# Kernel optimization log

Hardware: AMD Instinct MI355X
Metric: run time of the kernel (lower is better)

The kernel has to match this reference:

```python
import jax, jax.numpy as jnp
import numpy as np

B, T, E = 2, 4096, 768
H, Dh = 12, 64
W = 256  # one-sided window
GLOBAL_IDX = np.arange(0, 4096, 256)  # 16 global token positions
G = GLOBAL_IDX.shape[0]
NEG = -1e9


def setup_inputs() -> dict:
    key = jax.random.key(0)
    ks = jax.random.split(key, 13)
    p = lambda k, shape: jax.random.normal(k, shape, dtype=jnp.float32) * 0.02
    inp = {"x": jax.random.normal(ks[0], (B, T, E), dtype=jnp.float32)}
    for n_i, n in enumerate(["q", "k", "v", "qg", "kg", "vg"]):
        inp["W" + n] = p(ks[1 + 2 * n_i], (E, E))
        inp["b" + n] = p(ks[2 + 2 * n_i], (E,))
    return inp


def _heads(t):
    # [B,T,E] -> [B,H,T,Dh]
    return t.reshape(B, -1, H, Dh).transpose(0, 2, 1, 3)


def _chunk(t, w):
    # [B,H,T,d] -> [B,H,nc,3w,d]: key/value chunks covering [c*w - w, c*w + 2w)
    nc = T // w
    tp = jnp.pad(t, ((0, 0), (0, 0), (w, w), (0, 0)))
    idx = jnp.arange(nc)[:, None] * w + jnp.arange(3 * w)[None, :]
    return tp[:, :, idx, :]


def _forward(x, Wq, bq, Wk, bk, Wv, bv, Wqg, bqg, Wkg, bkg, Wvg, bvg):
    scale = 1.0 / np.sqrt(Dh)
    q = _heads(x @ Wq + bq) * scale
    k = _heads(x @ Wk + bk)
    v = _heads(x @ Wv + bv)
    nc = T // W
    qc = q.reshape(B, H, nc, W, Dh)
    kc = _chunk(k, W)
    vc = _chunk(v, W)
    # banded local scores via 3-chunk trick: [B,H,nc,W,3W]
    scores = jnp.einsum('bhcid,bhcjd->bhcij', qc, kc)
    i = jnp.arange(W)
    j = jnp.arange(3 * W)
    band = (j[None, :] >= i[:, None]) & (j[None, :] <= i[:, None] + 2 * W)  # |diff|<=W
    key_pos = jnp.arange(nc)[:, None] * W + j[None, :] - W  # [nc,3W] absolute key pos
    inseq = (key_pos >= 0) & (key_pos < T)
    valid = band[None] & inseq[:, None, :]  # [nc,W,3W]
    # remove global tokens from windowed attention (float -10000 mask, HF-style)
    is_glob = jnp.zeros((T,), jnp.float32).at[jnp.asarray(GLOBAL_IDX)].set(1.0)
    gmask = is_glob[jnp.clip(key_pos, 0, T - 1)] * inseq
    scores = scores - 10000.0 * gmask[None, None, :, None, :]
    scores = jnp.where(valid[None, None], scores, NEG)
    # every query also attends to global keys (local k/v projections gathered)
    k_glob = k[:, :, GLOBAL_IDX, :]  # [B,H,G,Dh]
    v_glob = v[:, :, GLOBAL_IDX, :]
    gscores = jnp.einsum('bhcid,bhgd->bhcig', qc, k_glob)  # [B,H,nc,W,G]
    allp = jax.nn.softmax(jnp.concatenate([gscores, scores], axis=-1), axis=-1)
    pg = allp[..., :G]
    pl = allp[..., G:] * valid[None, None]
    out = (jnp.einsum('bhcij,bhcjd->bhcid', pl, vc)
           + jnp.einsum('bhcig,bhgd->bhcid', pg, v_glob))
    out = out.reshape(B, H, T, Dh).transpose(0, 2, 1, 3).reshape(B, T, E)
    # global-query tokens: full attention with global projections, overwrite rows
    xg = x[:, GLOBAL_IDX, :]  # [B,G,E]
    qg = (xg @ Wqg + bqg).reshape(B, G, H, Dh).transpose(0, 2, 1, 3) * scale
    kgl = _heads(x @ Wkg + bkg)
    vgl = _heads(x @ Wvg + bvg)
    gp = jax.nn.softmax(jnp.einsum('bhgd,bhtd->bhgt', qg, kgl), axis=-1)
    go = jnp.einsum('bhgt,bhtd->bhgd', gp, vgl).transpose(0, 2, 1, 3).reshape(B, G, E)
    return out.at[:, GLOBAL_IDX, :].set(go)


def reference(x, Wq, bq, Wk, bk, Wv, bv, Wqg, bqg, Wkg, bkg, Wvg, bvg):
    return _forward(x, Wq, bq, Wk, bk, Wv, bv, Wqg, bqg, Wkg, bkg, Wvg, bvg)
```

## Files before the change

### kernel.cpp

```cpp
#include <hip/hip_runtime.h>
#include <stdint.h>
#include <stddef.h>

#define BB 2
#define TT 4096
#define EE 768
#define HH 12
#define DH 64
#define WW 256
#define NCHUNK 16
#define GG 16

typedef __bf16 bf16_t;
typedef __bf16 bf16x8 __attribute__((ext_vector_type(8)));
typedef float f32x4 __attribute__((ext_vector_type(4)));

__device__ inline f32x4 mfma16(bf16x8 a, bf16x8 b, f32x4 c) {
    return __builtin_amdgcn_mfma_f32_16x16x32_bf16(a, b, c, 0, 0, 0);
}

__device__ inline void gload16(const void* g, void* l) {
    __builtin_amdgcn_global_load_lds(
        (const __attribute__((address_space(1))) void*)g,
        (__attribute__((address_space(3))) void*)l, 16, 0, 0);
}

__global__ __launch_bounds__(256) void k_prep(const float* __restrict__ x,
                                              bf16_t* __restrict__ xb,
                                              const float* __restrict__ w0,
                                              const float* __restrict__ w1,
                                              const float* __restrict__ w2,
                                              const float* __restrict__ w3,
                                              const float* __restrict__ w4,
                                              bf16_t* __restrict__ wt) {
    __shared__ __align__(16) bf16_t ls[64 * 65];
    const int tid = threadIdx.x;
    if (blockIdx.x < 3072) {
        const int i = (blockIdx.x * 256 + tid) * 8;
        f32x4 a = *(const f32x4*)(x + i);
        f32x4 b = *(const f32x4*)(x + i + 4);
        bf16x8 o;
        o[0] = (bf16_t)a[0]; o[1] = (bf16_t)a[1]; o[2] = (bf16_t)a[2]; o[3] = (bf16_t)a[3];
        o[4] = (bf16_t)b[0]; o[5] = (bf16_t)b[1]; o[6] = (bf16_t)b[2]; o[7] = (bf16_t)b[3];
        *(bf16x8*)(xb + i) = o;
    } else {
        const int idx0 = blockIdx.x - 3072;
        const int z = idx0 / 144;
        const int rr = idx0 % 144;
        const int k0 = (rr / 12) * 64;
        const int n0 = (rr % 12) * 64;
        const float* W = (z == 0) ? w0 : (z == 1) ? w1 : (z == 2) ? w2 : (z == 3) ? w3 : w4;
        #pragma unroll
        for (int i = 0; i < 16; ++i) {
            int idx = i * 256 + tid;
            int kr = idx >> 6, nc = idx & 63;
            ls[nc * 65 + kr] = (bf16_t)W[(size_t)(k0 + kr) * EE + n0 + nc];
        }
        __syncthreads();
        bf16_t* o = wt + (size_t)z * EE * EE;
        #pragma unroll
        for (int i = 0; i < 16; ++i) {
            int idx = i * 256 + tid;
            int nr = idx >> 6, kc = idx & 63;
            o[(size_t)(n0 + nr) * EE + k0 + kc] = ls[nr * 65 + kc];
        }
    }
}

__global__ __launch_bounds__(256) void k_gemm(const bf16_t* __restrict__ xb,
                                              const bf16_t* __restrict__ wt,
                                              const float* __restrict__ b0,
                                              const float* __restrict__ b1,
                                              const float* __restrict__ b2,
                                              const float* __restrict__ b3,
                                              const float* __restrict__ b4,
                                              bf16_t* __restrict__ proj,
                                              bf16_t* __restrict__ vTp) {
    const int tid = threadIdx.x;
    const int z = blockIdx.z;
    const int m0 = blockIdx.x * 128;
    const int n0 = blockIdx.y * 128;
    const float* bias = (z == 0) ? b0 : (z == 1) ? b1 : (z == 2) ? b2 : (z == 3) ? b3 : b4;
    const float scale = (z == 0) ? 0.125f : 1.0f;
    const bf16_t* wz = wt + (size_t)z * EE * EE;
    bf16_t* dst = proj + (size_t)z * BB * HH * TT * DH;

    __shared__ __align__(16) char smem[65536];
    bf16_t* ct = (bf16_t*)smem;

    const int lane = tid & 63, wid = tid >> 6;
    const int wr = wid >> 1, wc = wid & 1;
    const int lg = lane >> 4, lr = lane & 15;
    const int srow = lane >> 3;
    const int scol = (lane & 7) * 8;

    f32x4 acc[4][4];
    const f32x4 z4 = {0.f, 0.f, 0.f, 0.f};
    #pragma unroll
    for (int i = 0; i < 4; ++i)
        #pragma unroll
        for (int j = 0; j < 4; ++j) acc[i][j] = z4;

    #pragma unroll
    for (int i = 0; i < 4; ++i) {
        const int seg = wid * 4 + i;
        const int row = seg * 8 + srow;
        gload16(xb + (size_t)(m0 + row) * EE + scol, smem + seg * 1024);
        gload16(wz + (size_t)(n0 + row) * EE + scol, smem + 16384 + seg * 1024);
    }
    __syncthreads();

    for (int kt = 0; kt < 12; ++kt) {
        const int cur = kt & 1;
        bf16_t* lA = (bf16_t*)(smem + cur * 32768);
        bf16_t* lB = (bf16_t*)(smem + cur * 32768 + 16384);

        if (kt < 11) {
            const int k0 = (kt + 1) * 64;
            char* nb = smem + (cur ^ 1) * 32768;
            #pragma unroll
            for (int i = 0; i < 4; ++i) {
                const int seg = wid * 4 + i;
                const int row = seg * 8 + srow;
                gload16(xb + (size_t)(m0 + row) * EE + k0 + scol, nb + seg * 1024);
                gload16(wz + (size_t)(n0 + row) * EE + k0 + scol, nb + 16384 + seg * 1024);
            }
        }

        #pragma unroll
        for (int kk = 0; kk < 2; ++kk) {
            bf16x8 af[4], bfr[4];
            #pragma unroll
            for (int mi = 0; mi < 4; ++mi)
                af[mi] = *(const bf16x8*)(&lA[(wr * 64 + mi * 16 + lr) * 64 + kk * 32 + lg * 8]);
            #pragma unroll
            for (int ni = 0; ni < 4; ++ni)
                bfr[ni] = *(const bf16x8*)(&lB[(wc * 64 + ni * 16 + lr) * 64 + kk * 32 + lg * 8]);
            #pragma unroll
            for (int mi = 0; mi < 4; ++mi)
                #pragma unroll
                for (int ni = 0; ni < 4; ++ni)
                    acc[mi][ni] = mfma16(af[mi], bfr[ni], acc[mi][ni]);
        }
        __syncthreads();
    }

    #pragma unroll
    for (int mi = 0; mi < 4; ++mi)
        #pragma unroll
        for (int ni = 0; ni < 4; ++ni) {
            const int nl = wc * 64 + ni * 16 + lr;
            const float bn = bias[n0 + nl];
            #pragma unroll
            for (int r = 0; r < 4; ++r) {
                const int ml_ = wr * 64 + mi * 16 + lg * 4 + r;
                ct[ml_ * 128 + nl] = (bf16_t)((acc[mi][ni][r] + bn) * scale);
            }
        }
    __syncthreads();

    if (z != 2) {
        #pragma unroll
        for (int it = 0; it < 8; ++it) {
            const int idx = it * 2048 + tid * 8;
            const int row = idx >> 7, col = idx & 127;
            const int m = m0 + row, n = n0 + col;
            const int h = n >> 6, d = n & 63;
            const int bb = m >> 12, t = m & 4095;
            *(bf16x8*)(dst + (((size_t)bb * HH + h) * TT + t) * DH + d) = *(const bf16x8*)(&ct[idx]);
        }
    } else {
        const int bb = m0 >> 12, tbase = m0 & 4095;
        #pragma unroll
        for (int it = 0; it < 8; ++it) {
            const int idx = it * 2048 + tid * 8;
            const int nl = idx >> 7;
            const int tp0 = idx & 127;
            const int h = (n0 + nl) >> 6, d = (n0 + nl) & 63;
            bf16x8 v;
            #pragma unroll
            for (int j = 0; j < 8; ++j) {
                const int tpl = tp0 + j;
                const int tau = tpl >> 6, s = tpl & 63;
                const int tl = tau * 64 + (s & 3) * 16 + (s >> 2);
                v[j] = ct[tl * 128 + nl];
            }
            *(bf16x8*)(vTp + (((size_t)bb * HH + h) * DH + d) * TT + tbase + tp0) = v;
        }
    }
}

__global__ __launch_bounds__(256) void k_attn(const bf16_t* __restrict__ qs,
                                              const bf16_t* __restrict__ ks,
                                              const bf16_t* __restrict__ vT,
                                              const float* __restrict__ x,
                                              const float* __restrict__ Wqg,
                                              const float* __restrict__ bqg,
                                              const bf16_t* __restrict__ kgl,
                                              const bf16_t* __restrict__ vgl,
                                              float* __restrict__ out) {
    __shared__ __align__(16) char smem[26880];
    const int tid = threadIdx.x;

    if (blockIdx.x < 1536) {
        const int gx0 = blockIdx.x;
        const int gx = (gx0 & 7) * 192 + (gx0 >> 3);
        const int q4 = gx & 3;
        const int c = (gx >> 2) & 15;
        const int bh = gx >> 6;
        const int b = bh / HH, h = bh % HH;
        const int w = tid >> 6;
        const int parity = w & 1;
        const int qbase = (w >> 1) * 32;
        const int lane = tid & 63, lg = lane >> 4, lr = lane & 15;

        const bf16_t* qp = qs + ((size_t)bh * TT + c * WW + q4 * 64 + qbase) * DH;
        const bf16_t* kp = ks + (size_t)bh * TT * DH;
        const bf16_t* vp = vT + (size_t)bh * DH * TT;

        bf16_t* Pw  = (bf16_t*)(smem + (size_t)w * 4608);
        bf16_t* Kg  = (bf16_t*)(smem + 18432);
        bf16_t* VgT = (bf16_t*)(smem + 20736);
        float*  ml  = (float*)(smem + 25856);
        float*  OmP = (float*)(smem + (size_t)(w >> 1) * 8192);

        if (w == 0) {
            #pragma unroll
            for (int i = 0; i < 2; ++i) {
                int idx = i * 64 + lane;
                int r = idx >> 3, d8 = (idx & 7) * 8;
                *(bf16x8*)(&Kg[r * 72 + d8]) = *(const bf16x8*)(kp + (size_t)r * WW * DH + d8);
            }
        } else if (w == 1) {
            #pragma unroll
            for (int g = 0; g < 32; ++g)
                VgT[lane * 40 + g] = (g < 16) ? vp[(size_t)lane * TT + g * WW] : (bf16_t)0.f;
        }

        bf16x8 Qf[2][2];
        #pragma unroll
        for (int mi = 0; mi < 2; ++mi)
            #pragma unroll
            for (int kk = 0; kk < 2; ++kk)
                Qf[mi][kk] = *(const bf16x8*)(qp + (size_t)(mi * 16 + lr) * DH + kk * 32 + lg * 8);

        f32x4 O[2][4];
        const f32x4 z4 = {0.f, 0.f, 0.f, 0.f};
        #pragma unroll
        for (int i = 0; i < 2; ++i)
            #pragma unroll
            for (int j = 0; j < 4; ++j) O[i][j] = z4;

        float m_own[8], l_own[8];
        #pragma unroll
        for (int i = 0; i < 8; ++i) { m_own[i] = -1e30f; l_own[i] = 0.f; }

        __syncthreads();

        for (int ts = parity; ts < 10; ts += 2) {
            const bool isg = (ts == 0);
            const int jt = q4 + ts - 1;
            const int ttile = 4 * (c - 1) + jt;
            if (!isg && (ttile < 0 || ttile > 63)) continue;
            const bool gdrop = !isg && ((jt & 3) == 0);
            const bool anymask = (ts == 1) || (ts == 9) || gdrop;

            bf16x8 kf[4][2];
            if (isg) {
                #pragma unroll
                for (int kk = 0; kk < 2; ++kk)
                    kf[0][kk] = *(const bf16x8*)(&Kg[lr * 72 + kk * 32 + lg * 8]);
            } else {
                const bf16_t* ktp = kp + (size_t)ttile * 64 * DH;
                #pragma unroll
                for (int ni = 0; ni < 4; ++ni)
                    #pragma unroll
                    for (int kk = 0; kk < 2; ++kk)
                        kf[ni][kk] = *(const bf16x8*)(ktp + (size_t)(ni * 16 + lr) * DH + kk * 32 + lg * 8);
            }

            #pragma unroll
            for (int mi = 0; mi < 2; ++mi) {
                f32x4 S[4] = {z4, z4, z4, z4};
                if (isg) {
                    #pragma unroll
                    for (int kk = 0; kk < 2; ++kk)
                        S[0] = mfma16(Qf[mi][kk], kf[0][kk], S[0]);
                } else {
                    #pragma unroll
                    for (int kk = 0; kk < 2; ++kk)
                        #pragma unroll
                        for (int ni = 0; ni < 4; ++ni)
                            S[ni] = mfma16(Qf[mi][kk], kf[ni][kk], S[ni]);
                }

                #pragma unroll
                for (int r = 0; r < 4; ++r) {
                    const int lrow = mi * 16 + lg * 4 + r;
                    const int row = qbase + lrow;
                    const int idx = mi * 4 + r;
                    float sv[4];
                    if (anymask || isg) {
                        #pragma unroll
                        for (int ni = 0; ni < 4; ++ni) {
                            const int cc = ni * 16 + lr;
                            bool ok = isg ? (ni == 0)
                                          : !((ts == 1 && cc < row) || (ts == 9 && cc > row) ||
                                              (gdrop && cc == 0));
                            sv[ni] = ok ? S[ni][r] : -1e30f;
                        }
                    } else {
                        #pragma unroll
                        for (int ni = 0; ni < 4; ++ni) sv[ni] = S[ni][r];
                    }
                    const float town = fmaxf(fmaxf(sv[0], sv[1]), fmaxf(sv[2], sv[3]));
                    if (!__all(town <= m_own[idx] + 8.f)) {
                        float tmax = town;
                        tmax = fmaxf(tmax, __shfl_xor(tmax, 1));
                        tmax = fmaxf(tmax, __shfl_xor(tmax, 2));
                        tmax = fmaxf(tmax, __shfl_xor(tmax, 4));
                        tmax = fmaxf(tmax, __shfl_xor(tmax, 8));
                        const float m2 = fmaxf(m_own[idx], tmax);
                        const float scr = __expf(m_own[idx] - m2);
                        m_own[idx] = m2;
                        l_own[idx] *= scr;
                        #pragma unroll
                        for (int di = 0; di < 4; ++di) O[mi][di][r] *= scr;
                    }
                    const float p0 = __expf(sv[0] - m_own[idx]);
                    const float p1 = __expf(sv[1] - m_own[idx]);
                    const float p2 = __expf(sv[2] - m_own[idx]);
                    const float p3 = __expf(sv[3] - m_own[idx]);
                    l_own[idx] += (p0 + p1) + (p2 + p3);
                    if (isg) {
                        Pw[lrow * 72 + 0 * 16 + lr] = (bf16_t)p0;
                        Pw[lrow * 72 + 1 * 16 + lr] = (bf16_t)p1;
                        Pw[lrow * 72 + 2 * 16 + lr] = (bf16_t)p2;
                        Pw[lrow * 72 + 3 * 16 + lr] = (bf16_t)p3;
                    } else {
                        uint32_t d0, d1;
                        asm("v_cvt_pk_bf16_f32 %0, %1, %2" : "=v"(d0) : "v"(p0), "v"(p1));
                        asm("v_cvt_pk_bf16_f32 %0, %1, %2" : "=v"(d1) : "v"(p2), "v"(p3));
                        uint32_t* dstp = (uint32_t*)(&Pw[lrow * 72 + lr * 4]);
                        dstp[0] = d0;
                        dstp[1] = d1;
                    }
                }
            }

            asm volatile("s_waitcnt lgkmcnt(0)" ::: "memory");
            __builtin_amdgcn_sched_barrier(0);

            #pragma unroll
            for (int kkp = 0; kkp < 2; ++kkp) {
                if (isg && kkp == 1) continue;
                bf16x8 pa[2];
                #pragma unroll
                for (int mi = 0; mi < 2; ++mi)
                    pa[mi] = *(const bf16x8*)(&Pw[(mi * 16 + lr) * 72 + kkp * 32 + lg * 8]);
                #pragma unroll
                for (int di = 0; di < 4; ++di) {
                    bf16x8 vf;
                    if (isg)
                        vf = *(const bf16x8*)(&VgT[(di * 16 + lr) * 40 + lg * 8]);
                    else
                        vf = *(const bf16x8*)(vp + (size_t)(di * 16 + lr) * TT + ttile * 64 + kkp * 32 + lg * 8);
                    #pragma unroll
                    for (int mi = 0; mi < 2; ++mi) O[mi][di] = mfma16(pa[mi], vf, O[mi][di]);
                }
            }
        }

        #pragma unroll
        for (int i = 0; i < 8; ++i) {
            float l = l_own[i];
            l += __shfl_xor(l, 1);
            l += __shfl_xor(l, 2);
            l += __shfl_xor(l, 4);
            l += __shfl_xor(l, 8);
            l_own[i] = l;
        }

        #pragma unroll
        for (int mi = 0; mi < 2; ++mi)
            #pragma unroll
            for (int r = 0; r < 4; ++r)
                if (lr == 0) {
                    int lrow = mi * 16 + lg * 4 + r;
                    ml[w * 64 + lrow]      = m_own[mi * 4 + r];
                    ml[w * 64 + 32 + lrow] = l_own[mi * 4 + r];
                }
        __syncthreads();

        if (parity) {
            #pragma unroll
            for (int mi = 0; mi < 2; ++mi)
                #pragma unroll
                for (int r = 0; r < 4; ++r) {
                    const int lrow = mi * 16 + lg * 4 + r;
                    const int idx = mi * 4 + r;
                    const float mstar = fmaxf(ml[(w - 1) * 64 + lrow], m_own[idx]);
                    const float s1 = __expf(m_own[idx] - mstar);
                    #pragma unroll
                    for (int di = 0; di < 4; ++di)
                        OmP[lrow * 64 + di * 16 + lr] = O[mi][di][r] * s1;
                    if (lr == 0) ml[w * 64 + 32 + lrow] = l_own[idx] * s1;
                }
        }
        __syncthreads();

        if (!parity) {
            const bool gskip = (q4 == 0) && (qbase == 0);
            const size_t outbase = ((size_t)b * TT + c * WW + q4 * 64 + qbase) * EE + h * DH;
            #pragma unroll
            for (int mi = 0; mi < 2; ++mi)
                #pragma unroll
                for (int r = 0; r < 4; ++r) {
                    const int lrow = mi * 16 + lg * 4 + r;
                    const int idx = mi * 4 + r;
                    const float m1 = ml[(w + 1) * 64 + lrow];
                    const float mstar = fmaxf(m_own[idx], m1);
                    const float s0 = __expf(m_own[idx] - mstar);
                    const float l = l_own[idx] * s0 + ml[(w + 1) * 64 + 32 + lrow];
                    const float linv = 1.f / l;
                    if (gskip && lrow == 0) continue;
                    #pragma unroll
                    for (int di = 0; di < 4; ++di)
                        out[outbase + (size_t)lrow * EE + di * 16 + lr] =
                            (O[mi][di][r] * s0 + OmP[lrow * 64 + di * 16 + lr]) * linv;
                }
        }
    } else {
        const int gx0 = blockIdx.x - 1536;
        const int xcd = gx0 & 7, y = gx0 >> 3;
        const int bh = xcd * 3 + (y >> 4);
        const int g = y & 15;
        const int b = bh / HH, h = bh % HH;
        const int lane = tid & 63, w = tid >> 6;

        float* qrow = (float*)smem;
        float* sc   = (float*)(smem + 256);
        float* red  = (float*)(smem + 16640);
        float* xr   = (float*)(smem + 17664);

        const float* xrow = x + ((size_t)b * TT + g * WW) * EE;
        for (int i = tid; i < EE; i += 256) xr[i] = xrow[i];
        __syncthreads();
        {
            const int d = tid & 63;
            const int e0 = (tid >> 6) * 192;
            float p = 0.f;
            for (int e = e0; e < e0 + 192; ++e)
                p += xr[e] * Wqg[(size_t)e * EE + h * DH + d];
            red[tid] = p;
        }
        __syncthreads();
        if (tid < DH)
            qrow[tid] = (red[tid] + red[64 + tid] + red[128 + tid] + red[192 + tid]
                         + bqg[h * DH + tid]) * 0.125f;
        __syncthreads();

        const bf16_t* kp = kgl + (size_t)bh * TT * DH;
        float lmax = -1e30f;
        for (int t = tid; t < TT; t += 256) {
            const bf16_t* kr = kp + (size_t)t * DH;
            float s = 0.f;
            #pragma unroll
            for (int d0 = 0; d0 < DH; d0 += 8) {
                bf16x8 kv = *(const bf16x8*)(kr + d0);
                #pragma unroll
                for (int jj = 0; jj < 8; ++jj) s += qrow[d0 + jj] * (float)kv[jj];
            }
            sc[t] = s;
            lmax = fmaxf(lmax, s);
        }
        #pragma unroll
        for (int off = 32; off; off >>= 1) lmax = fmaxf(lmax, __shfl_xor(lmax, off));
        if (lane == 0) red[w] = lmax;
        __syncthreads();
        const float M = fmaxf(fmaxf(red[0], red[1]), fmaxf(red[2], red[3]));
        float lsum = 0.f;
        for (int t = tid; t < TT; t += 256) {
            float p = __expf(sc[t] - M);
            sc[t] = p;
            lsum += p;
        }
        #pragma unroll
        for (int off = 32; off; off >>= 1) lsum += __shfl_xor(lsum, off);
        __syncthreads();
        if (lane == 0) red[64 + w] = lsum;
        __syncthreads();
        const float SUM = red[64] + red[65] + red[66] + red[67];
        __syncthreads();

        const bf16_t* vp = vgl + (size_t)bh * TT * DH;
        const int rq = lane >> 3, dq = (lane & 7) * 8;
        float a[8];
        #pragma unroll
        for (int j = 0; j < 8; ++j) a[j] = 0.f;
        const int tbase = w * 1024;
        #pragma unroll 4
        for (int i = 0; i < 128; ++i) {
            const int t = tbase + rq + 8 * i;
            const float s = sc[t];
            bf16x8 vv = *(const bf16x8*)(vp + (size_t)t * DH + dq);
            #pragma unroll
            for (int j = 0; j < 8; ++j) a[j] += s * (float)vv[j];
        }
        #pragma unroll
        for (int j = 0; j < 8; ++j) {
            float v = a[j];
            v += __shfl_xor(v, 8);
            v += __shfl_xor(v, 16);
            v += __shfl_xor(v, 32);
            a[j] = v;
        }
        if (rq == 0) {
            #pragma unroll
            for (int j = 0; j < 8; ++j) red[w * 64 + dq + j] = a[j];
        }
        __syncthreads();
        if (w == 0) {
            float tot = red[lane] + red[64 + lane] + red[128 + lane] + red[192 + lane];
            out[((size_t)b * TT + g * WW) * EE + h * DH + lane] = tot / SUM;
        }
    }
}

extern "C" void kernel_launch(void* const* d_in, const int* in_sizes, int n_in,
                              void* d_out, int out_size, void* d_ws, size_t ws_size,
                              hipStream_t stream) {
    const float* x   = (const float*)d_in[0];
    const float* Wq  = (const float*)d_in[1];
    const float* bq  = (const float*)d_in[2];
    const float* Wk  = (const float*)d_in[3];
    const float* bk  = (const float*)d_in[4];
    const float* Wv  = (const float*)d_in[5];
    const float* bv  = (const float*)d_in[6];
    const float* Wqg = (const float*)d_in[7];
    const float* bqg = (const float*)d_in[8];
    const float* Wkg = (const float*)d_in[9];
    const float* bkg = (const float*)d_in[10];
    const float* Wvg = (const float*)d_in[11];
    const float* bvg = (const float*)d_in[12];
    float* out = (float*)d_out;

    const size_t NX = (size_t)BB * TT * EE;
    const size_t NW = (size_t)EE * EE;
    const size_t NP = (size_t)BB * HH * TT * DH;

    bf16_t* xb   = (bf16_t*)d_ws;
    bf16_t* wt   = xb + NX;
    bf16_t* proj = wt + 5 * NW;
    bf16_t* vT   = proj + 5 * NP;

    (void)bvg; (void)in_sizes; (void)n_in; (void)out_size; (void)ws_size;

    k_prep<<<dim3(3792), 256, 0, stream>>>(x, xb, Wq, Wk, Wv, Wkg, Wvg, wt);
    k_gemm<<<dim3(64, 6, 5), 256, 0, stream>>>(xb, wt, bq, bk, bv, bkg, bvg, proj, vT);
    k_attn<<<dim3(1920), 256, 0, stream>>>(proj, proj + NP, vT, x, Wqg, bqg,
                                           proj + 3 * NP, proj + 4 * NP, out);
}
```

Measured before the change: 215.2 us.

## Split global-query attention over key range with a separate combine kernel

Global-token attention blocks now each handle one quarter of the key sequence (split-K/flash-decoding style). They write partial max, sum and output to a workspace buffer, and a new small kernel merges the four partials with rescaling. This raises the global-query blocks from 384 to 1536, shortening that tail of the attention kernel, and shrinks per-block shared memory. In exchange it adds an extra kernel launch, workspace traffic, and recomputes the q projection four times per global row.

```diff
diff --git a/kernel.cpp b/kernel.cpp
--- a/kernel.cpp
+++ b/kernel.cpp
@@ -198,6 +198,7 @@
                                               const float* __restrict__ bqg,
                                               const bf16_t* __restrict__ kgl,
                                               const bf16_t* __restrict__ vgl,
+                                              float* __restrict__ part,
                                               float* __restrict__ out) {
     __shared__ __align__(16) char smem[26880];
     const int tid = threadIdx.x;
@@ -433,15 +434,18 @@
     } else {
         const int gx0 = blockIdx.x - 1536;
         const int xcd = gx0 & 7, y = gx0 >> 3;
-        const int bh = xcd * 3 + (y >> 4);
-        const int g = y & 15;
+        const int uix = y >> 2;
+        const int piece = y & 3;
+        const int bh = xcd * 3 + (uix >> 4);
+        const int g = uix & 15;
         const int b = bh / HH, h = bh % HH;
+        const int t0 = piece * 1024;
         const int lane = tid & 63, w = tid >> 6;
 
         float* qrow = (float*)smem;
         float* sc   = (float*)(smem + 256);
-        float* red  = (float*)(smem + 16640);
-        float* xr   = (float*)(smem + 17664);
+        float* red  = (float*)(smem + 4608);
+        float* xr   = (float*)(smem + 5632);
 
         const float* xrow = x + ((size_t)b * TT + g * WW) * EE;
         for (int i = tid; i < EE; i += 256) xr[i] = xrow[i];
@@ -461,8 +465,11 @@
         __syncthreads();
 
         const bf16_t* kp = kgl + (size_t)bh * TT * DH;
+        float s_acc[4];
         float lmax = -1e30f;
-        for (int t = tid; t < TT; t += 256) {
+        #pragma unroll
+        for (int i = 0; i < 4; ++i) {
+            const int t = t0 + tid + 256 * i;
             const bf16_t* kr = kp + (size_t)t * DH;
             float s = 0.f;
             #pragma unroll
@@ -471,7 +478,7 @@
                 #pragma unroll
                 for (int jj = 0; jj < 8; ++jj) s += qrow[d0 + jj] * (float)kv[jj];
             }
-            sc[t] = s;
+            s_acc[i] = s;
             lmax = fmaxf(lmax, s);
         }
         #pragma unroll
@@ -480,9 +487,10 @@
         __syncthreads();
         const float M = fmaxf(fmaxf(red[0], red[1]), fmaxf(red[2], red[3]));
         float lsum = 0.f;
-        for (int t = tid; t < TT; t += 256) {
-            float p = __expf(sc[t] - M);
-            sc[t] = p;
+        #pragma unroll
+        for (int i = 0; i < 4; ++i) {
+            float p = __expf(s_acc[i] - M);
+            sc[tid + 256 * i] = p;
             lsum += p;
         }
         #pragma unroll
@@ -498,12 +506,12 @@
         float a[8];
         #pragma unroll
         for (int j = 0; j < 8; ++j) a[j] = 0.f;
-        const int tbase = w * 1024;
+        const int tb = w * 256;
         #pragma unroll 4
-        for (int i = 0; i < 128; ++i) {
-            const int t = tbase + rq + 8 * i;
-            const float s = sc[t];
-            bf16x8 vv = *(const bf16x8*)(vp + (size_t)t * DH + dq);
+        for (int i = 0; i < 32; ++i) {
+            const int tl = tb + rq + 8 * i;
+            const float s = sc[tl];
+            bf16x8 vv = *(const bf16x8*)(vp + (size_t)(t0 + tl) * DH + dq);
             #pragma unroll
             for (int j = 0; j < 8; ++j) a[j] += s * (float)vv[j];
         }
@@ -521,10 +529,28 @@
         }
         __syncthreads();
         if (w == 0) {
-            float tot = red[lane] + red[64 + lane] + red[128 + lane] + red[192 + lane];
-            out[((size_t)b * TT + g * WW) * EE + h * DH + lane] = tot / SUM;
+            float* slot = part + ((size_t)(bh * GG + g) * 4 + piece) * 68;
+            float o = red[lane] + red[64 + lane] + red[128 + lane] + red[192 + lane];
+            slot[2 + lane] = o;
+            if (lane == 0) { slot[0] = M; slot[1] = SUM; }
         }
     }
+}
+
+__global__ __launch_bounds__(64) void k_fin(const float* __restrict__ part,
+                                            float* __restrict__ out) {
+    const int u = blockIdx.x;
+    const int bh = u >> 4, g = u & 15;
+    const int b = bh / HH, h = bh % HH;
+    const int d = threadIdx.x;
+    const float* s = part + (size_t)u * 4 * 68;
+    const float m0 = s[0], m1 = s[68], m2 = s[136], m3 = s[204];
+    const float ms = fmaxf(fmaxf(m0, m1), fmaxf(m2, m3));
+    const float e0 = __expf(m0 - ms), e1 = __expf(m1 - ms);
+    const float e2 = __expf(m2 - ms), e3 = __expf(m3 - ms);
+    const float l = s[1] * e0 + s[69] * e1 + s[137] * e2 + s[205] * e3;
+    const float o = s[2 + d] * e0 + s[70 + d] * e1 + s[138 + d] * e2 + s[206 + d] * e3;
+    out[((size_t)b * TT + g * WW) * EE + h * DH + d] = o / l;
 }
 
 extern "C" void kernel_launch(void* const* d_in, const int* in_sizes, int n_in,
@@ -553,11 +579,13 @@
     bf16_t* wt   = xb + NX;
     bf16_t* proj = wt + 5 * NW;
     bf16_t* vT   = proj + 5 * NP;
+    float*  part = (float*)(vT + NP);
 
     (void)bvg; (void)in_sizes; (void)n_in; (void)out_size; (void)ws_size;
 
     k_prep<<<dim3(3792), 256, 0, stream>>>(x, xb, Wq, Wk, Wv, Wkg, Wvg, wt);
     k_gemm<<<dim3(64, 6, 5), 256, 0, stream>>>(xb, wt, bq, bk, bv, bkg, bvg, proj, vT);
-    k_attn<<<dim3(1920), 256, 0, stream>>>(proj, proj + NP, vT, x, Wqg, bqg,
-                                           proj + 3 * NP, proj + 4 * NP, out);
-}
+    k_attn<<<dim3(3072), 256, 0, stream>>>(proj, proj + NP, vT, x, Wqg, bqg,
+                                           proj + 3 * NP, proj + 4 * NP, part, out);
+    k_fin<<<dim3(384), 64, 0, stream>>>(part, out);
+}
```

After: 223.7 us. 4.0% more time.
